# Kernel tuning notes

Hardware: AMD Instinct MI355X
Metric: run time of the kernel (lower is better)

Reference implementation:

```python
import jax, jax.numpy as jnp
import numpy as np

N_NODES = 100000
N_EDGES = 1600000
IN_FEAT = 128
HEADS = 4
OUT_FEAT = 16
ALPHA = 0.2  # LeakyReLU negative slope


def setup_inputs() -> dict:
    key = jax.random.key(0)
    k1, k2, k3, k4, k5 = jax.random.split(key, 5)
    x = jax.random.normal(k1, (N_NODES, IN_FEAT), dtype=jnp.float32)
    edge_index = jax.random.randint(k2, (2, N_EDGES), 0, N_NODES, dtype=jnp.int64)
    # xavier_uniform with gain=1.414
    gain = 1.414
    lim_W = gain * np.sqrt(6.0 / (IN_FEAT + HEADS * OUT_FEAT))
    W = jax.random.uniform(k3, (IN_FEAT, HEADS * OUT_FEAT), minval=-lim_W, maxval=lim_W, dtype=jnp.float32)
    lim_a = gain * np.sqrt(6.0 / (HEADS + OUT_FEAT))
    a_src = jax.random.uniform(k4, (HEADS, OUT_FEAT), minval=-lim_a, maxval=lim_a, dtype=jnp.float32)
    a_dst = jax.random.uniform(k5, (HEADS, OUT_FEAT), minval=-lim_a, maxval=lim_a, dtype=jnp.float32)
    return {"x": x, "edge_index": edge_index, "W": W, "a_src": a_src, "a_dst": a_dst}


def reference(x, edge_index, W, a_src, a_dst):
    N = x.shape[0]
    H, F = a_src.shape
    src, dst = edge_index[0], edge_index[1]

    h = (x @ W).reshape(N, H, F)                 # [N, H, F]
    att_src = jnp.sum(h * a_src, axis=-1)        # [N, H]
    att_dst = jnp.sum(h * a_dst, axis=-1)        # [N, H]

    e = jax.nn.leaky_relu(att_src[src] + att_dst[dst], negative_slope=ALPHA)  # [E, H]

    # segment softmax over edges grouped by dst
    e_max = jax.ops.segment_max(e, dst, num_segments=N)   # [N, H]
    e_max = jnp.where(jnp.isfinite(e_max), e_max, 0.0)    # nodes with no in-edges
    ex = jnp.exp(e - e_max[dst])                           # [E, H]
    denom = jax.ops.segment_sum(ex, dst, num_segments=N)  # [N, H]
    alpha = ex / (denom[dst] + 1e-16)                      # [E, H]
    # dropout: inference mode (training=False) -> identity

    messages = h[src] * alpha[:, :, None]                  # [E, H, F]
    out = jax.ops.segment_sum(messages, dst, num_segments=N)  # [N, H, F]

    out = out.reshape(N, H * F)  # concat=True
    out = jax.nn.elu(out)
    return out
```

## Files before the change

### kernel.cpp

```cpp
#include <hip/hip_runtime.h>


#define NEG_SLOPE 0.2f
#define BSHIFT 9
#define BNODES 512
#define CH 2048
#define QNODES 64
#define BCAP 9216
#define SCAP 1536

typedef __bf16 bf16x8 __attribute__((ext_vector_type(8)));
typedef float  f32x4  __attribute__((ext_vector_type(4)));

static __device__ __forceinline__ unsigned f2b(float f) {
    union { float f; unsigned u; } v; v.f = f;
    return (v.u + 0x7fffu + ((v.u >> 16) & 1u)) >> 16;
}
static __device__ __forceinline__ float u2f(unsigned u) {
    union { unsigned u32; float f; } v; v.u32 = u; return v.f;
}

__global__ __launch_bounds__(256) void gemm_att_kernel(
    const float* __restrict__ x,
    const float* __restrict__ W,
    const float* __restrict__ a_src,
    const float* __restrict__ a_dst,
    unsigned short* __restrict__ h_out,
    float* __restrict__ att_s_o,
    float* __restrict__ att_d_o,
    int N)
{
    __shared__ bf16x8 Wswz[20][64];
    int t = threadIdx.x;

    for (int i = t; i < 8192; i += 256) {
        int k = i >> 6, n = i & 63;
        __bf16* dp = (__bf16*)&Wswz[((n >> 4) << 2) | (k >> 5)]
                                   [(((k >> 3) & 3) << 4) | (n & 15)];
        dp[k & 7] = (__bf16)W[i];
    }
    for (int i = t; i < 1024; i += 256) {
        int k = i >> 3, c7 = i & 7;
        int hd = c7 & 3;
        const float* aa = (c7 < 4) ? a_src : a_dst;
        float sum = 0.f;
        #pragma unroll
        for (int f = 0; f < 16; ++f)
            sum = fmaf(W[k * 64 + hd * 16 + f], aa[hd * 16 + f], sum);
        __bf16* dp = (__bf16*)&Wswz[16 + (k >> 5)][(((k >> 3) & 3) << 4) | c7];
        dp[k & 7] = (__bf16)sum;
        __bf16* dz = (__bf16*)&Wswz[16 + (k >> 5)][(((k >> 3) & 3) << 4) | (8 + c7)];
        dz[k & 7] = (__bf16)0.f;
    }
    __syncthreads();

    int wave = t >> 6;
    int lane = t & 63;
    int col = lane & 15, quad = lane >> 4;
    int node_base = (blockIdx.x * 4 + wave) * 16;
    int arow = min(node_base + col, N - 1);
    const float* xp = x + arow * 128;

    bf16x8 af[4];
    #pragma unroll
    for (int tt = 0; tt < 4; ++tt) {
        float4 xa = *(const float4*)(xp + tt * 32 + quad * 8);
        float4 xb = *(const float4*)(xp + tt * 32 + quad * 8 + 4);
        bf16x8 f;
        f[0] = (__bf16)xa.x; f[1] = (__bf16)xa.y;
        f[2] = (__bf16)xa.z; f[3] = (__bf16)xa.w;
        f[4] = (__bf16)xb.x; f[5] = (__bf16)xb.y;
        f[6] = (__bf16)xb.z; f[7] = (__bf16)xb.w;
        af[tt] = f;
    }

    f32x4 acc[4], accA;
    #pragma unroll
    for (int cb = 0; cb < 4; ++cb) {
        acc[cb] = (f32x4){0.f, 0.f, 0.f, 0.f};
        #pragma unroll
        for (int tt = 0; tt < 4; ++tt)
            acc[cb] = __builtin_amdgcn_mfma_f32_16x16x32_bf16(
                af[tt], Wswz[(cb << 2) | tt][lane], acc[cb], 0, 0, 0);
    }
    accA = (f32x4){0.f, 0.f, 0.f, 0.f};
    #pragma unroll
    for (int tt = 0; tt < 4; ++tt)
        accA = __builtin_amdgcn_mfma_f32_16x16x32_bf16(
            af[tt], Wswz[16 + tt][lane], accA, 0, 0, 0);

    #pragma unroll
    for (int cb = 0; cb < 4; ++cb) {
        #pragma unroll
        for (int r = 0; r < 4; ++r) {
            int node = node_base + quad * 4 + r;
            if (node < N)
                h_out[node * 64 + cb * 16 + col] = (unsigned short)f2b(acc[cb][r]);
        }
    }
    if (col < 8) {
        #pragma unroll
        for (int r = 0; r < 4; ++r) {
            int node = node_base + quad * 4 + r;
            if (node < N) {
                if (col < 4) att_s_o[(node << 2) | col] = accA[r];
                else         att_d_o[(node << 2) | (col - 4)] = accA[r];
            }
        }
    }
}

__global__ __launch_bounds__(256) void bscatter_kernel(
    const int* __restrict__ src, const int* __restrict__ dst,
    int* __restrict__ gcur, int* __restrict__ pairs, int E)
{
    __shared__ int cnt[256], lo[256], gpos[256], cur[256], sm[256];
    __shared__ int2 staged[CH];
    int t = threadIdx.x;
    int base = blockIdx.x * CH;
    int nloc = min(CH, E - base);

    cnt[t] = 0;
    __syncthreads();
    for (int i = t; i < nloc; i += 256)
        atomicAdd(&cnt[dst[base + i] >> BSHIFT], 1);
    __syncthreads();

    int v = cnt[t];
    sm[t] = v;
    __syncthreads();
    #pragma unroll
    for (int off = 1; off < 256; off <<= 1) {
        int u = (t >= off) ? sm[t - off] : 0;
        __syncthreads();
        sm[t] += u;
        __syncthreads();
    }
    lo[t] = sm[t] - v;
    cur[t] = lo[t];
    gpos[t] = (v > 0) ? t * BCAP + atomicAdd(&gcur[t], v) : 0;
    __syncthreads();

    for (int i = t; i < nloc; i += 256) {
        int d = dst[base + i];
        int s = src[base + i];
        int b = d >> BSHIFT;
        int k = atomicAdd(&cur[b], 1);
        staged[k] = make_int2((s << BSHIFT) | (d & (BNODES - 1)), b);
    }
    __syncthreads();

    for (int i = t; i < nloc; i += 256) {
        int2 p = staged[i];
        int pos = gpos[p.y] + (i - lo[p.y]);
        if (pos < (p.y + 1) * BCAP)
            pairs[pos] = p.x;
    }
}

__global__ __launch_bounds__(256) void sliceshuffle_kernel(
    const int* __restrict__ pairs, const int* __restrict__ gcur,
    int* __restrict__ pairs2, int* __restrict__ scur)
{
    int blk = blockIdx.x, t = threadIdx.x;
    int b = blk >> 3, chunk = blk & 7;
    int cnt = min(gcur[b], BCAP);
    int clo = (cnt * chunk) >> 3;
    int chi = (cnt * (chunk + 1)) >> 3;
    int lane = t & 63;
    unsigned long long below = (lane == 0) ? 0ull : ((~0ull) >> (64 - lane));
    const int* pb = pairs + (size_t)b * BCAP;

    for (int i = clo + t; i < chi; i += 256) {
        int p = pb[i];
        int sl = (p >> 6) & 7;
        int pos = 0;
        #pragma unroll
        for (int s = 0; s < 8; ++s) {
            unsigned long long m = __ballot(sl == s);
            if (sl == s) {
                int rank = __popcll(m & below);
                int b0 = 0;
                if (rank == 0)
                    b0 = atomicAdd(&scur[(b << 3) | s], (int)__popcll(m));
                b0 = __shfl(b0, (int)(__ffsll((long long)m) - 1), 64);
                pos = b0 + rank;
            }
        }
        if (pos < SCAP)
            pairs2[(size_t)((b << 3) | sl) * SCAP + pos] = p;
    }
}

__global__ __launch_bounds__(256, 8) void bucket_csr_agg_kernel(
    const int* __restrict__ pairs2,
    const int* __restrict__ scur,
    const float* __restrict__ att_s,
    const float* __restrict__ att_d,
    const unsigned short* __restrict__ hmat,
    float* __restrict__ out,
    int N)
{
    __shared__ int sorted[SCAP];
    __shared__ int cnt[QNODES], rs[QNODES + 1], cur[QNODES], sm[QNODES];
    __shared__ float attd[QNODES * 4];

    int blk = blockIdx.x, t = threadIdx.x;
    int b = blk >> 3, s8 = blk & 7;
    int node_lo = (b << BSHIFT) + (s8 << 6);
    if (node_lo >= N) return;
    int nn = min(QNODES, N - node_lo);

    int ebase = blk * SCAP;
    int ecnt  = min(scur[blk], SCAP);

    if (t < QNODES) cnt[t] = 0;
    for (int i = t; i < (nn << 2); i += 256)
        attd[i] = att_d[(node_lo << 2) + i];
    __syncthreads();

    for (int i = t; i < ecnt; i += 256)
        atomicAdd(&cnt[pairs2[ebase + i] & (QNODES - 1)], 1);
    __syncthreads();

    int v = (t < QNODES) ? cnt[t] : 0;
    if (t < QNODES) sm[t] = v;
    __syncthreads();
    #pragma unroll
    for (int off = 1; off < QNODES; off <<= 1) {
        int u = (t >= off && t < QNODES) ? sm[t - off] : 0;
        __syncthreads();
        if (t < QNODES) sm[t] += u;
        __syncthreads();
    }
    if (t < QNODES) {
        int x = sm[t] - v; rs[t] = x; cur[t] = x;
        if (t == QNODES - 1) rs[QNODES] = sm[t];
    }
    __syncthreads();

    for (int i = t; i < ecnt; i += 256) {
        int p = pairs2[ebase + i];
        int k = atomicAdd(&cur[p & (QNODES - 1)], 1);
        if (k < SCAP) sorted[k] = p >> BSHIFT;
    }
    __syncthreads();

    int q = t & 7;
    int h = q >> 1;
    int nclamp = N - 1;

    for (int pass = 0; pass < 2; ++pass) {
        int node = (pass << 5) + (t >> 3);
        if (node >= nn) continue;
        int beg = rs[node];
        int deg = rs[node + 1] - beg;
        float ad = attd[(node << 2) | h];

        float a0 = 0.f, a1 = 0.f, a2 = 0.f, a3 = 0.f;
        float a4 = 0.f, a5 = 0.f, a6 = 0.f, a7 = 0.f, l = 0.f;
        int d1 = deg - 1;
        for (int e0 = 0; e0 < deg; e0 += 4) {
            int s0 = min(sorted[beg + min(e0 + 0, d1)], nclamp);
            int s1 = min(sorted[beg + min(e0 + 1, d1)], nclamp);
            int s2 = min(sorted[beg + min(e0 + 2, d1)], nclamp);
            int s3 = min(sorted[beg + min(e0 + 3, d1)], nclamp);
            float t0 = att_s[(s0 << 2) | h];
            float t1 = att_s[(s1 << 2) | h];
            float t2 = att_s[(s2 << 2) | h];
            float t3 = att_s[(s3 << 2) | h];
            uint4 hp0 = *(const uint4*)(hmat + (s0 << 6) + (q << 3));
            uint4 hp1 = *(const uint4*)(hmat + (s1 << 6) + (q << 3));
            uint4 hp2 = *(const uint4*)(hmat + (s2 << 6) + (q << 3));
            uint4 hp3 = *(const uint4*)(hmat + (s3 << 6) + (q << 3));
            float av0 = t0 + ad; av0 = fmaxf(av0, NEG_SLOPE * av0);
            float av1 = t1 + ad; av1 = fmaxf(av1, NEG_SLOPE * av1);
            float av2 = t2 + ad; av2 = fmaxf(av2, NEG_SLOPE * av2);
            float av3 = t3 + ad; av3 = fmaxf(av3, NEG_SLOPE * av3);
            float w0 = __expf(av0);
            float w1 = (e0 + 1 < deg) ? __expf(av1) : 0.f;
            float w2 = (e0 + 2 < deg) ? __expf(av2) : 0.f;
            float w3 = (e0 + 3 < deg) ? __expf(av3) : 0.f;
            l += w0 + w1 + w2 + w3;
            a0 = fmaf(w0, u2f(hp0.x << 16), a0);
            a1 = fmaf(w0, u2f(hp0.x & 0xffff0000u), a1);
            a2 = fmaf(w0, u2f(hp0.y << 16), a2);
            a3 = fmaf(w0, u2f(hp0.y & 0xffff0000u), a3);
            a4 = fmaf(w0, u2f(hp0.z << 16), a4);
            a5 = fmaf(w0, u2f(hp0.z & 0xffff0000u), a5);
            a6 = fmaf(w0, u2f(hp0.w << 16), a6);
            a7 = fmaf(w0, u2f(hp0.w & 0xffff0000u), a7);
            a0 = fmaf(w1, u2f(hp1.x << 16), a0);
            a1 = fmaf(w1, u2f(hp1.x & 0xffff0000u), a1);
            a2 = fmaf(w1, u2f(hp1.y << 16), a2);
            a3 = fmaf(w1, u2f(hp1.y & 0xffff0000u), a3);
            a4 = fmaf(w1, u2f(hp1.z << 16), a4);
            a5 = fmaf(w1, u2f(hp1.z & 0xffff0000u), a5);
            a6 = fmaf(w1, u2f(hp1.w << 16), a6);
            a7 = fmaf(w1, u2f(hp1.w & 0xffff0000u), a7);
            a0 = fmaf(w2, u2f(hp2.x << 16), a0);
            a1 = fmaf(w2, u2f(hp2.x & 0xffff0000u), a1);
            a2 = fmaf(w2, u2f(hp2.y << 16), a2);
            a3 = fmaf(w2, u2f(hp2.y & 0xffff0000u), a3);
            a4 = fmaf(w2, u2f(hp2.z << 16), a4);
            a5 = fmaf(w2, u2f(hp2.z & 0xffff0000u), a5);
            a6 = fmaf(w2, u2f(hp2.w << 16), a6);
            a7 = fmaf(w2, u2f(hp2.w & 0xffff0000u), a7);
            a0 = fmaf(w3, u2f(hp3.x << 16), a0);
            a1 = fmaf(w3, u2f(hp3.x & 0xffff0000u), a1);
            a2 = fmaf(w3, u2f(hp3.y << 16), a2);
            a3 = fmaf(w3, u2f(hp3.y & 0xffff0000u), a3);
            a4 = fmaf(w3, u2f(hp3.z << 16), a4);
            a5 = fmaf(w3, u2f(hp3.z & 0xffff0000u), a5);
            a6 = fmaf(w3, u2f(hp3.w << 16), a6);
            a7 = fmaf(w3, u2f(hp3.w & 0xffff0000u), a7);
        }

        float rl = 1.0f / (l + 1e-16f);
        float4 v0, v1;
        v0.x = a0 * rl; v0.x = (v0.x > 0.f) ? v0.x : (__expf(v0.x) - 1.f);
        v0.y = a1 * rl; v0.y = (v0.y > 0.f) ? v0.y : (__expf(v0.y) - 1.f);
        v0.z = a2 * rl; v0.z = (v0.z > 0.f) ? v0.z : (__expf(v0.z) - 1.f);
        v0.w = a3 * rl; v0.w = (v0.w > 0.f) ? v0.w : (__expf(v0.w) - 1.f);
        v1.x = a4 * rl; v1.x = (v1.x > 0.f) ? v1.x : (__expf(v1.x) - 1.f);
        v1.y = a5 * rl; v1.y = (v1.y > 0.f) ? v1.y : (__expf(v1.y) - 1.f);
        v1.z = a6 * rl; v1.z = (v1.z > 0.f) ? v1.z : (__expf(v1.z) - 1.f);
        v1.w = a7 * rl; v1.w = (v1.w > 0.f) ? v1.w : (__expf(v1.w) - 1.f);
        float* op = out + ((size_t)(node_lo + node) << 6) + (q << 3);
        *(float4*)op = v0;
        *(float4*)(op + 4) = v1;
    }
}

extern "C" void kernel_launch(void* const* d_in, const int* in_sizes, int n_in,
                              void* d_out, int out_size, void* d_ws, size_t ws_size,
                              hipStream_t stream) {
    const float* x     = (const float*)d_in[0];
    const int*   ei    = (const int*)d_in[1];
    const float* W     = (const float*)d_in[2];
    const float* a_src = (const float*)d_in[3];
    const float* a_dst = (const float*)d_in[4];

    int N = in_sizes[0] / 128;
    int E = in_sizes[1] / 2;
    const int* src = ei;
    const int* dst = ei + E;
    int nb = (N + BNODES - 1) / BNODES;

    char* ws = (char*)d_ws;
    size_t off = 0;
    unsigned short* hmat = (unsigned short*)(ws + off); off += (size_t)N * 64 * 2;
    float* att_s = (float*)(ws + off);  off += (size_t)N * 4 * 4;
    float* att_d = (float*)(ws + off);  off += (size_t)N * 4 * 4;
    int* pairs    = (int*)(ws + off);   off += (size_t)nb * BCAP * 4;
    int* pairs2   = (int*)(ws + off);   off += (size_t)nb * 8 * SCAP * 4;
    int* gcur     = (int*)(ws + off);   off += 256 * 4;
    int* scur     = (int*)(ws + off);   off += (size_t)nb * 8 * 4;

    hipMemsetAsync(gcur, 0, (256 + nb * 8) * 4, stream);

    int gemmBlocks = (N + 63) / 64;
    gemm_att_kernel<<<gemmBlocks, 256, 0, stream>>>(
        x, W, a_src, a_dst, hmat, att_s, att_d, N);

    int blocksS = (E + CH - 1) / CH;
    bscatter_kernel<<<blocksS, 256, 0, stream>>>(src, dst, gcur, pairs, E);

    sliceshuffle_kernel<<<nb * 8, 256, 0, stream>>>(pairs, gcur, pairs2, scur);

    bucket_csr_agg_kernel<<<nb * 8, 256, 0, stream>>>(
        pairs2, scur, att_s, att_d, hmat, (float*)d_out, N);
}
```

Baseline: 233.3 us.

## Replace global slice atomics with per-block LDS counters and chunked segments

The slice shuffle now gives each block private per-chunk output segments and counts them with LDS atomics, so it no longer contends on global atomic counters. The aggregation kernel reads the eight chunk segments per slice using the stored counts. Zeroing gcur moves into the GEMM kernel, which removes the hipMemsetAsync call. The cost is a fixed per-chunk cap of 256 edges, which could drop edges on heavily skewed inputs, and extra loop overhead in the aggregation kernel.

```diff
diff --git a/kernel.cpp b/kernel.cpp
--- a/kernel.cpp
+++ b/kernel.cpp
@@ -8,6 +8,7 @@
 #define QNODES 64
 #define BCAP 9216
 #define SCAP 1536
+#define SCAPC 256
 
 typedef __bf16 bf16x8 __attribute__((ext_vector_type(8)));
 typedef float  f32x4  __attribute__((ext_vector_type(4)));
@@ -28,10 +29,13 @@
     unsigned short* __restrict__ h_out,
     float* __restrict__ att_s_o,
     float* __restrict__ att_d_o,
+    int* __restrict__ gcur,
     int N)
 {
     __shared__ bf16x8 Wswz[20][64];
     int t = threadIdx.x;
+
+    if (blockIdx.x == 0) gcur[t] = 0;
 
     for (int i = t; i < 8192; i += 256) {
         int k = i >> 6, n = i & 63;
@@ -160,8 +164,9 @@
 
 __global__ __launch_bounds__(256) void sliceshuffle_kernel(
     const int* __restrict__ pairs, const int* __restrict__ gcur,
-    int* __restrict__ pairs2, int* __restrict__ scur)
+    int* __restrict__ pairs2, int* __restrict__ scnt)
 {
+    __shared__ int cur8[8];
     int blk = blockIdx.x, t = threadIdx.x;
     int b = blk >> 3, chunk = blk & 7;
     int cnt = min(gcur[b], BCAP);
@@ -170,6 +175,8 @@
     int lane = t & 63;
     unsigned long long below = (lane == 0) ? 0ull : ((~0ull) >> (64 - lane));
     const int* pb = pairs + (size_t)b * BCAP;
+    if (t < 8) cur8[t] = 0;
+    __syncthreads();
 
     for (int i = clo + t; i < chi; i += 256) {
         int p = pb[i];
@@ -181,20 +188,21 @@
             if (sl == s) {
                 int rank = __popcll(m & below);
                 int b0 = 0;
-                if (rank == 0)
-                    b0 = atomicAdd(&scur[(b << 3) | s], (int)__popcll(m));
+                if (rank == 0) b0 = atomicAdd(&cur8[s], (int)__popcll(m));
                 b0 = __shfl(b0, (int)(__ffsll((long long)m) - 1), 64);
                 pos = b0 + rank;
             }
         }
-        if (pos < SCAP)
-            pairs2[(size_t)((b << 3) | sl) * SCAP + pos] = p;
-    }
+        if (pos < SCAPC)
+            pairs2[((size_t)((((b << 3) | sl) << 3) | chunk)) * SCAPC + pos] = p;
+    }
+    __syncthreads();
+    if (t < 8) scnt[((((b << 3) | t) << 3) | chunk)] = min(cur8[t], SCAPC);
 }
 
 __global__ __launch_bounds__(256, 8) void bucket_csr_agg_kernel(
     const int* __restrict__ pairs2,
-    const int* __restrict__ scur,
+    const int* __restrict__ scnt,
     const float* __restrict__ att_s,
     const float* __restrict__ att_d,
     const unsigned short* __restrict__ hmat,
@@ -203,6 +211,7 @@
 {
     __shared__ int sorted[SCAP];
     __shared__ int cnt[QNODES], rs[QNODES + 1], cur[QNODES], sm[QNODES];
+    __shared__ int scn[8];
     __shared__ float attd[QNODES * 4];
 
     int blk = blockIdx.x, t = threadIdx.x;
@@ -211,16 +220,20 @@
     if (node_lo >= N) return;
     int nn = min(QNODES, N - node_lo);
 
-    int ebase = blk * SCAP;
-    int ecnt  = min(scur[blk], SCAP);
-
     if (t < QNODES) cnt[t] = 0;
+    if (t < 8) scn[t] = scnt[(blk << 3) | t];
     for (int i = t; i < (nn << 2); i += 256)
         attd[i] = att_d[(node_lo << 2) + i];
     __syncthreads();
 
-    for (int i = t; i < ecnt; i += 256)
-        atomicAdd(&cnt[pairs2[ebase + i] & (QNODES - 1)], 1);
+    const int* sbase = pairs2 + ((size_t)blk << 3) * SCAPC;
+    #pragma unroll
+    for (int c = 0; c < 8; ++c) {
+        int cn = scn[c];
+        const int* seg = sbase + c * SCAPC;
+        for (int i = t; i < cn; i += 256)
+            atomicAdd(&cnt[seg[i] & (QNODES - 1)], 1);
+    }
     __syncthreads();
 
     int v = (t < QNODES) ? cnt[t] : 0;
@@ -239,10 +252,15 @@
     }
     __syncthreads();
 
-    for (int i = t; i < ecnt; i += 256) {
-        int p = pairs2[ebase + i];
-        int k = atomicAdd(&cur[p & (QNODES - 1)], 1);
-        if (k < SCAP) sorted[k] = p >> BSHIFT;
+    #pragma unroll
+    for (int c = 0; c < 8; ++c) {
+        int cn = scn[c];
+        const int* seg = sbase + c * SCAPC;
+        for (int i = t; i < cn; i += 256) {
+            int p = seg[i];
+            int k = atomicAdd(&cur[p & (QNODES - 1)], 1);
+            if (k < SCAP) sorted[k] = p >> BSHIFT;
+        }
     }
     __syncthreads();
 
@@ -353,21 +371,19 @@
     float* att_s = (float*)(ws + off);  off += (size_t)N * 4 * 4;
     float* att_d = (float*)(ws + off);  off += (size_t)N * 4 * 4;
     int* pairs    = (int*)(ws + off);   off += (size_t)nb * BCAP * 4;
-    int* pairs2   = (int*)(ws + off);   off += (size_t)nb * 8 * SCAP * 4;
+    int* pairs2   = (int*)(ws + off);   off += (size_t)nb * 64 * SCAPC * 4;
     int* gcur     = (int*)(ws + off);   off += 256 * 4;
-    int* scur     = (int*)(ws + off);   off += (size_t)nb * 8 * 4;
-
-    hipMemsetAsync(gcur, 0, (256 + nb * 8) * 4, stream);
+    int* scnt     = (int*)(ws + off);   off += (size_t)nb * 64 * 4;
 
     int gemmBlocks = (N + 63) / 64;
     gemm_att_kernel<<<gemmBlocks, 256, 0, stream>>>(
-        x, W, a_src, a_dst, hmat, att_s, att_d, N);
+        x, W, a_src, a_dst, hmat, att_s, att_d, gcur, N);
 
     int blocksS = (E + CH - 1) / CH;
     bscatter_kernel<<<blocksS, 256, 0, stream>>>(src, dst, gcur, pairs, E);
 
-    sliceshuffle_kernel<<<nb * 8, 256, 0, stream>>>(pairs, gcur, pairs2, scur);
+    sliceshuffle_kernel<<<nb * 8, 256, 0, stream>>>(pairs, gcur, pairs2, scnt);
 
     bucket_csr_agg_kernel<<<nb * 8, 256, 0, stream>>>(
-        pairs2, scur, att_s, att_d, hmat, (float*)d_out, N);
-}
+        pairs2, scnt, att_s, att_d, hmat, (float*)d_out, N);
+}
```

New measurement: 201.5 us. 13.6% less time.
